# Kernel optimization log

Hardware: AMD Instinct MI355X
Metric: run time of the kernel (lower is better)

Reference implementation:

```python
import jax, jax.numpy as jnp
import numpy as np

BN_EPS = 1e-3  # keras BatchNormalization default epsilon

def _prelu(x, a):
    return jnp.maximum(x, 0) + a * jnp.minimum(x, 0)

def _bn(x, g, b, m, v):
    # inference-mode batchnorm with moving statistics
    return (x - m) * jax.lax.rsqrt(v + BN_EPS) * g + b

def setup_inputs() -> dict:
    key = jax.random.key(0)
    ks = jax.random.split(key, 24)
    B, D, V, L = 4096, 768, 200000, 200000
    F = 3 * D  # 2304 = qid|pos|neg concat
    n = lambda i, shape, s=0.05: jax.random.normal(ks[i], shape, jnp.float32) * s
    return dict(
        qid_embeddings=jax.random.normal(ks[0], (B, D), jnp.float32),
        node_embeddings=n(1, (V, D), 0.1),
        leaf_embeddings=n(2, (L, D), 0.1),
        positives=jax.random.randint(ks[3], (B,), 0, V),
        negetives=jax.random.randint(ks[4], (B,), 0, V),
        p_isleafs=jax.random.randint(ks[5], (B,), 0, 2),
        n_isleafs=jax.random.randint(ks[6], (B,), 0, 2),
        W00=n(7, (F, 36)), b00=jnp.zeros((36,)), a00=jnp.full((36,), 0.25),
        W01=n(8, (36, 1)), b01=jnp.zeros((1,)),
        W1=n(9, (F, 128)), b1=jnp.zeros((128,)), a1=jnp.full((128,), 0.25),
        g1=jnp.ones((128,)), be1=n(10, (128,), 0.1), m1=n(11, (128,), 0.1),
        v1=jax.random.uniform(ks[12], (128,)) + 0.5,
        W2=n(13, (128, 64)), b2=jnp.zeros((64,)), a2=jnp.full((64,), 0.25),
        g2=jnp.ones((64,)), be2=n(14, (64,), 0.1), m2=n(15, (64,), 0.1),
        v2=jax.random.uniform(ks[16], (64,)) + 0.5,
        W3=n(17, (64, 24)), b3=jnp.zeros((24,)), a3=jnp.full((24,), 0.25),
        g3=jnp.ones((24,)), be3=n(18, (24,), 0.1), m3=n(19, (24,), 0.1),
        v3=jax.random.uniform(ks[20], (24,)) + 0.5,
        W4=n(21, (24, 2)), b4=jnp.zeros((2,)),
    )

def reference(qid_embeddings, node_embeddings, leaf_embeddings, positives, negetives,
              p_isleafs, n_isleafs, W00, b00, a00, W01, b01,
              W1, b1, a1, g1, be1, m1, v1,
              W2, b2, a2, g2, be2, m2, v2,
              W3, b3, a3, g3, be3, m3, v3, W4, b4):
    # per-sample conditional embedding gather (leaf table vs internal node table)
    pos = jnp.where((p_isleafs == 1)[:, None], leaf_embeddings[positives], node_embeddings[positives])  # [B,D]
    neg = jnp.where((n_isleafs == 1)[:, None], leaf_embeddings[negetives], node_embeddings[negetives])  # [B,D]
    q = qid_embeddings  # [B,D]
    # attention block: small Dense(36)->Dense(1) scalar weight per sample
    feat = jnp.concatenate([q, pos, neg], axis=1)  # [B,3D]
    h = _prelu(feat @ W00 + b00, a00)              # [B,36]
    w = h @ W01 + b01                              # [B,1]
    item = jnp.concatenate([w * pos, w * neg, q], axis=1)  # [B,3D]
    # MLP 2304 -> 128 -> 64 -> 24 -> 2 (layer10/20/30 unused in original call)
    x = _bn(_prelu(item @ W1 + b1, a1), g1, be1, m1, v1)
    x = _bn(_prelu(x @ W2 + b2, a2), g2, be2, m2, v2)
    x = _bn(_prelu(x @ W3 + b3, a3), g3, be3, m3, v3)
    return jax.nn.softmax(x @ W4 + b4, axis=-1)  # [B,2]
```

## Files before the change

### kernel.cpp

```cpp
#include <hip/hip_runtime.h>
#include <hip/hip_bf16.h>

typedef _Float16 half8 __attribute__((ext_vector_type(8)));
typedef _Float16 half4v __attribute__((ext_vector_type(4)));
typedef float f32x4 __attribute__((ext_vector_type(4)));

#define NCOLS 176
#define TILE_ELEMS (NCOLS*32)
#define TILE_U16 (TILE_ELEMS/8)
#define WTSTR 40
#define XSTR2 2312
#define BM 16

#define BAR() do { asm volatile("s_waitcnt lgkmcnt(0)" ::: "memory"); \
  __builtin_amdgcn_s_barrier(); \
  __builtin_amdgcn_sched_barrier(0); } while (0)

#define OFF_A36 0
#define OFF_TQ  2560
#define OFF_TPN 10752
#define OFF_WV  18944
#define OFF_X1  19008
#define OFF_W2  27456
#define OFF_X2  43840
#define OFF_W3  48192
#define OFF_X3  51264
#define OFF_SCR 53056
#define SM_BYTES 77632

struct Params {
  const float *qid, *node, *leaf;
  const int *pos_idx, *neg_idx, *p_leaf, *n_leaf;
  const float *b00, *a00, *W01, *b01;
  const float *b1, *a1, *g1, *be1, *m1, *v1;
  const float *W2, *b2, *a2, *g2, *be2, *m2, *v2;
  const float *W3, *b3, *a3, *g3, *be3, *m3, *v3;
  const float *W4, *b4;
  const _Float16 *Wp;
  float *out;
};

__global__ __launch_bounds__(256) void pack_weights(const float* __restrict__ W00,
                                                    const float* __restrict__ W1,
                                                    _Float16* __restrict__ Wp) {
  int g = blockIdx.x;
  int s = g / 24, t = g - s * 24;
  int k0 = t * 32;
  int w1row0 = (s == 0) ? 1536 : (s == 1 ? 0 : 768);
  __shared__ _Float16 T[NCOLS][WTSTR];
  int tid = threadIdx.x;
  for (int u = tid; u < 1024; u += 256) {
    int kk = u >> 5, c4 = u & 31;
    float4 f = *(const float4*)(W1 + (size_t)(w1row0 + k0 + kk) * 128 + c4 * 4);
    int c = 48 + c4 * 4;
    T[c + 0][kk] = (_Float16)f.x; T[c + 1][kk] = (_Float16)f.y;
    T[c + 2][kk] = (_Float16)f.z; T[c + 3][kk] = (_Float16)f.w;
  }
  for (int u = tid; u < 1152; u += 256) {
    int kk = u / 36, c = u - kk * 36;
    T[c][kk] = (_Float16)W00[(size_t)(s * 768 + k0 + kk) * 36 + c];
  }
  for (int u = tid; u < 384; u += 256) {
    int kk = u & 31, c = 36 + (u >> 5);
    T[c][kk] = (_Float16)0.f;
  }
  __syncthreads();
  uint4* dst = (uint4*)(Wp + (size_t)g * TILE_ELEMS);
  for (int u = tid; u < TILE_U16; u += 256) {
    int c = u >> 2, q = u & 3;
    dst[u] = *(const uint4*)&T[c][q * 8];
  }
}

__global__ __launch_bounds__(512) void fused_main(Params p) {
  __shared__ __align__(16) char sm[SM_BYTES];
  __shared__ const float* Xbase[3][BM];

  _Float16* X   = (_Float16*)sm;
  float*    A36 = (float*)(sm + OFF_A36);
  float*    Tq  = (float*)(sm + OFF_TQ);
  float*    Tpn = (float*)(sm + OFF_TPN);
  float*    wv  = (float*)(sm + OFF_WV);
  float*    x1  = (float*)(sm + OFF_X1);
  _Float16* W2h = (_Float16*)(sm + OFF_W2);
  float*    x2  = (float*)(sm + OFF_X2);
  _Float16* W3h = (_Float16*)(sm + OFF_W3);
  float*    x3  = (float*)(sm + OFF_X3);
  float*    scr = (float*)(sm + OFF_SCR);

  const int tid  = threadIdx.x;
  const int wid  = tid >> 6;
  const int lane = tid & 63;
  const int lm   = lane & 15;
  const int hk   = lane >> 4;
  const int nw   = wid & 3;
  const int kg   = wid >> 2;
  const int m0   = blockIdx.x * BM;
  const bool HAS2 = (nw < 3);

  const uint4* Wp4 = (const uint4*)p.Wp;
  const int woff = ((nw * 48 + lm) << 2) + hk;

  uint4 P[4][3];
  auto ldWp = [&](int j) {
    int s = j / 12;
    int g = s * 24 + kg + 2 * (j - s * 12);
    const uint4* b = Wp4 + (size_t)g * TILE_U16 + woff;
    P[j & 3][0] = b[0]; P[j & 3][1] = b[64];
    if (HAS2) P[j & 3][2] = b[128];
  };

  ldWp(0); ldWp(1); ldWp(2); ldWp(3);

  if (tid < 3 * BM) {
    int s = tid >> 4, i = tid & 15;
    const float* base;
    if (s == 0) base = p.qid + (size_t)(m0 + i) * 768;
    else if (s == 1) {
      int idx = p.pos_idx[m0 + i];
      base = ((p.p_leaf[m0 + i] == 1) ? p.leaf : p.node) + (size_t)idx * 768;
    } else {
      int idx = p.neg_idx[m0 + i];
      base = ((p.n_leaf[m0 + i] == 1) ? p.leaf : p.node) + (size_t)idx * 768;
    }
    Xbase[s][i] = base;
  }

  float4 sregA[6], sregB[6], sregC[6];
  auto stageLoad = [&](int s, float4* sr) {
#pragma unroll
    for (int jj = 0; jj < 6; ++jj) {
      int v = tid + jj * 512;
      int i = v / 192, c4 = v - i * 192;
      const float* b = (s == 0) ? (p.qid + (size_t)(m0 + i) * 768) : Xbase[s][i];
      sr[jj] = ((const float4*)b)[c4];
    }
  };
  auto stageWrite = [&](int s, const float4* sr) {
#pragma unroll
    for (int jj = 0; jj < 6; ++jj) {
      int v = tid + jj * 512;
      int i = v / 192, c4 = v - i * 192;
      float4 f = sr[jj];
      half4v h = { (_Float16)f.x, (_Float16)f.y, (_Float16)f.z, (_Float16)f.w };
      *(half4v*)(X + i * XSTR2 + s * 768 + c4 * 4) = h;
    }
  };

  BAR();
  stageLoad(0, sregA);
  stageLoad(1, sregB);
  stageLoad(2, sregC);
  stageWrite(0, sregA);
  BAR();

  f32x4 accA[3] = {{0.f,0.f,0.f,0.f},{0.f,0.f,0.f,0.f},{0.f,0.f,0.f,0.f}};
  f32x4 accB[3] = {{0.f,0.f,0.f,0.f},{0.f,0.f,0.f,0.f},{0.f,0.f,0.f,0.f}};
  half8 av[3];

  auto ldA = [&](int g) -> half8 {
    return *(const half8*)(X + lm * XSTR2 + g * 32 + hk * 8);
  };
  auto comp = [&](int g, int slot, half8 a) {
    half8 b0 = __builtin_bit_cast(half8, P[slot][0]);
    half8 b1 = __builtin_bit_cast(half8, P[slot][1]);
    half8 b2 = __builtin_bit_cast(half8, P[slot][2]);
    if ((nw == 0) || (g < 24)) {
      accA[0] = __builtin_amdgcn_mfma_f32_16x16x32_f16(a, b0, accA[0], 0, 0, 0);
      accA[1] = __builtin_amdgcn_mfma_f32_16x16x32_f16(a, b1, accA[1], 0, 0, 0);
      if (HAS2) accA[2] = __builtin_amdgcn_mfma_f32_16x16x32_f16(a, b2, accA[2], 0, 0, 0);
    } else {
      accB[0] = __builtin_amdgcn_mfma_f32_16x16x32_f16(a, b0, accB[0], 0, 0, 0);
      accB[1] = __builtin_amdgcn_mfma_f32_16x16x32_f16(a, b1, accB[1], 0, 0, 0);
      if (HAS2) accB[2] = __builtin_amdgcn_mfma_f32_16x16x32_f16(a, b2, accB[2], 0, 0, 0);
    }
  };

  float4 w2r[4];
#pragma unroll
  for (int s = 0; s < 3; ++s) {
    if (s == 1) {
#pragma unroll
      for (int jj = 0; jj < 4; ++jj) w2r[jj] = ((const float4*)p.W2)[tid + jj * 512];
      stageWrite(1, sregB);
      BAR();
    }
    if (s == 2) {
      stageWrite(2, sregC);
      BAR();
    }
    const int gb = s * 24 + kg;
    av[0] = ldA(gb); av[1] = ldA(gb + 2); av[2] = ldA(gb + 4);
#pragma unroll
    for (int tt = 0; tt < 12; ++tt) {
      int j = s * 12 + tt;
      comp(gb + 2 * tt, j & 3, av[tt % 3]);
      if (j + 4 < 36) ldWp(j + 4);
      if (tt + 3 < 12) av[tt % 3] = ldA(gb + 2 * (tt + 3));
    }
  }

  BAR();
  if (kg == 1) {
#pragma unroll
    for (int n = 0; n < 3; ++n) {
      if (n < 2 || HAS2) {
#pragma unroll
        for (int r = 0; r < 4; ++r) {
          int base = ((nw * 3 + n) * 2) * 256 + (hk * 4 + r) * 16 + lm;
          scr[base]       = accA[n][r];
          scr[base + 256] = accB[n][r];
        }
      }
    }
  }
  BAR();
  if (kg == 0) {
#pragma unroll
    for (int n = 0; n < 3; ++n) {
      if (n < 2 || HAS2) {
#pragma unroll
        for (int r = 0; r < 4; ++r) {
          int base = ((nw * 3 + n) * 2) * 256 + (hk * 4 + r) * 16 + lm;
          float va = accA[n][r] + scr[base];
          float vb = accB[n][r] + scr[base + 256];
          int row = hk * 4 + r;
          int col = nw * 48 + n * 16 + lm;
          if (nw == 0) { if (col < 36) A36[row * 40 + col] = va; }
          else { int rc = col - 48; Tq[row * 128 + rc] = va; Tpn[row * 128 + rc] = vb; }
        }
      }
    }
  }
  BAR();

#pragma unroll
  for (int jj = 0; jj < 4; ++jj) {
    int u = tid + jj * 512;
    float4 f = w2r[jj];
    half4v h = { (_Float16)f.x, (_Float16)f.y, (_Float16)f.z, (_Float16)f.w };
    *(half4v*)(W2h + (u >> 4) * 64 + (u & 15) * 4) = h;
  }
  if (tid < BM) {
    float acc = p.b01[0];
    for (int c = 0; c < 36; ++c) {
      float h = A36[tid * 40 + c] + p.b00[c];
      h = (h > 0.f) ? h : p.a00[c] * h;
      acc += h * p.W01[c];
    }
    wv[tid] = acc;
  }
  BAR();

#pragma unroll
  for (int j = 0; j < 4; ++j) {
    int u = tid + j * 512;
    int i = u >> 7, c = u & 127;
    float v = wv[i] * Tpn[i * 128 + c] + Tq[i * 128 + c] + p.b1[c];
    v = (v > 0.f) ? v : p.a1[c] * v;
    v = (v - p.m1[c]) * (1.f / sqrtf(p.v1[c] + 1e-3f)) * p.g1[c] + p.be1[c];
    x1[i * 132 + c] = v;
  }
  BAR();

  if (tid < 256) {
    int i = tid & 15, cq = tid >> 4;
    const float* xr = x1 + i * 132;
    f32x4 acc0 = { p.b2[cq*4+0], p.b2[cq*4+1], p.b2[cq*4+2], p.b2[cq*4+3] };
    f32x4 acc1 = { 0.f, 0.f, 0.f, 0.f };
#pragma unroll 8
    for (int k = 0; k < 128; k += 2) {
      half4v w0 = *(const half4v*)(W2h + k * 64 + cq * 4);
      half4v w1 = *(const half4v*)(W2h + (k + 1) * 64 + cq * 4);
      acc0 += xr[k]     * __builtin_convertvector(w0, f32x4);
      acc1 += xr[k + 1] * __builtin_convertvector(w1, f32x4);
    }
    f32x4 acc = acc0 + acc1;
#pragma unroll
    for (int jj = 0; jj < 4; ++jj) {
      int c = cq * 4 + jj;
      float v = acc[jj];
      v = (v > 0.f) ? v : p.a2[c] * v;
      v = (v - p.m2[c]) * (1.f / sqrtf(p.v2[c] + 1e-3f)) * p.g2[c] + p.be2[c];
      x2[i * 68 + c] = v;
    }
  }
  for (int j = 0; j < 3; ++j) {
    int u = tid + j * 512;
    W3h[u] = (_Float16)p.W3[u];
  }
  BAR();

  if (tid < 384) {
    int i = tid & 15, c = tid >> 4;
    float acc = p.b3[c];
#pragma unroll 8
    for (int k = 0; k < 64; ++k) acc += x2[i * 68 + k] * (float)W3h[k * 24 + c];
    acc = (acc > 0.f) ? acc : p.a3[c] * acc;
    acc = (acc - p.m3[c]) * (1.f / sqrtf(p.v3[c] + 1e-3f)) * p.g3[c] + p.be3[c];
    x3[i * 28 + c] = acc;
  }
  BAR();

  if (tid < BM) {
    float l0 = p.b4[0], l1 = p.b4[1];
#pragma unroll
    for (int k = 0; k < 24; ++k) {
      float v = x3[tid * 28 + k];
      l0 += v * p.W4[k * 2 + 0];
      l1 += v * p.W4[k * 2 + 1];
    }
    float m = fmaxf(l0, l1);
    float e0 = __expf(l0 - m), e1 = __expf(l1 - m);
    float inv = 1.f / (e0 + e1);
    p.out[(size_t)(m0 + tid) * 2 + 0] = e0 * inv;
    p.out[(size_t)(m0 + tid) * 2 + 1] = e1 * inv;
  }
}

extern "C" void kernel_launch(void* const* d_in, const int* in_sizes, int n_in,
                              void* d_out, int out_size, void* d_ws, size_t ws_size,
                              hipStream_t stream) {
  const float* qid  = (const float*)d_in[0];
  const float* node = (const float*)d_in[1];
  const float* leaf = (const float*)d_in[2];
  const int* positives = (const int*)d_in[3];
  const int* negetives = (const int*)d_in[4];
  const int* p_isleafs = (const int*)d_in[5];
  const int* n_isleafs = (const int*)d_in[6];
  const float* W00 = (const float*)d_in[7];
  const float* b00 = (const float*)d_in[8];
  const float* a00 = (const float*)d_in[9];
  const float* W01 = (const float*)d_in[10];
  const float* b01 = (const float*)d_in[11];
  const float* W1  = (const float*)d_in[12];
  const float* b1  = (const float*)d_in[13];
  const float* a1  = (const float*)d_in[14];
  const float* g1  = (const float*)d_in[15];
  const float* be1 = (const float*)d_in[16];
  const float* m1  = (const float*)d_in[17];
  const float* v1  = (const float*)d_in[18];
  const float* W2  = (const float*)d_in[19];
  const float* b2  = (const float*)d_in[20];
  const float* a2  = (const float*)d_in[21];
  const float* g2  = (const float*)d_in[22];
  const float* be2 = (const float*)d_in[23];
  const float* m2  = (const float*)d_in[24];
  const float* v2  = (const float*)d_in[25];
  const float* W3  = (const float*)d_in[26];
  const float* b3  = (const float*)d_in[27];
  const float* a3  = (const float*)d_in[28];
  const float* g3  = (const float*)d_in[29];
  const float* be3 = (const float*)d_in[30];
  const float* m3  = (const float*)d_in[31];
  const float* v3  = (const float*)d_in[32];
  const float* W4  = (const float*)d_in[33];
  const float* b4  = (const float*)d_in[34];

  _Float16* Wp = (_Float16*)d_ws;

  pack_weights<<<72, 256, 0, stream>>>(W00, W1, Wp);

  Params p;
  p.qid = qid; p.node = node; p.leaf = leaf;
  p.pos_idx = positives; p.neg_idx = negetives; p.p_leaf = p_isleafs; p.n_leaf = n_isleafs;
  p.b00 = b00; p.a00 = a00; p.W01 = W01; p.b01 = b01;
  p.b1 = b1; p.a1 = a1; p.g1 = g1; p.be1 = be1; p.m1 = m1; p.v1 = v1;
  p.W2 = W2; p.b2 = b2; p.a2 = a2; p.g2 = g2; p.be2 = be2; p.m2 = m2; p.v2 = v2;
  p.W3 = W3; p.b3 = b3; p.a3 = a3; p.g3 = g3; p.be3 = be3; p.m3 = m3; p.v3 = v3;
  p.W4 = W4; p.b4 = b4;
  p.Wp = Wp;
  p.out = (float*)d_out;

  int B = in_sizes[3];
  fused_main<<<B / BM, 512, 0, stream>>>(p);
}
```

Baseline: 41.18 us.

## Use 768 threads with 3-way K split and double-buffered activation staging

Raises the block size from 512 to 768 threads, so each of three K-groups handles one third of the fused GEMM K range instead of two halves. The staged q/pos/neg rows go into two ping-pong LDS buffers and the next segment is written while the current one computes. The shared pointer table and the leading barrier are removed, and the sched_barrier is dropped from BAR. Fewer per-thread registers and more concurrent waves are meant to hide gather latency, at the cost of more LDS per block (which may lower occupancy) and an extra cross-group reduction.

```diff
diff --git a/kernel.cpp b/kernel.cpp
--- a/kernel.cpp
+++ b/kernel.cpp
@@ -9,12 +9,13 @@
 #define TILE_ELEMS (NCOLS*32)
 #define TILE_U16 (TILE_ELEMS/8)
 #define WTSTR 40
-#define XSTR2 2312
+#define XSTR 776
+#define XBUF_F16 12416
 #define BM 16
+#define NTHR 768
 
 #define BAR() do { asm volatile("s_waitcnt lgkmcnt(0)" ::: "memory"); \
-  __builtin_amdgcn_s_barrier(); \
-  __builtin_amdgcn_sched_barrier(0); } while (0)
+  __builtin_amdgcn_s_barrier(); } while (0)
 
 #define OFF_A36 0
 #define OFF_TQ  2560
@@ -25,8 +26,8 @@
 #define OFF_X2  43840
 #define OFF_W3  48192
 #define OFF_X3  51264
-#define OFF_SCR 53056
-#define SM_BYTES 77632
+#define OFF_SCR 49664
+#define SM_BYTES 98816
 
 struct Params {
   const float *qid, *node, *leaf;
@@ -72,9 +73,8 @@
   }
 }
 
-__global__ __launch_bounds__(512) void fused_main(Params p) {
+__global__ __launch_bounds__(NTHR) void fused_main(Params p) {
   __shared__ __align__(16) char sm[SM_BYTES];
-  __shared__ const float* Xbase[3][BM];
 
   _Float16* X   = (_Float16*)sm;
   float*    A36 = (float*)(sm + OFF_A36);
@@ -103,8 +103,8 @@
 
   uint4 P[4][3];
   auto ldWp = [&](int j) {
-    int s = j / 12;
-    int g = s * 24 + kg + 2 * (j - s * 12);
+    int s = j >> 3;
+    int g = s * 24 + kg + 3 * (j - s * 8);
     const uint4* b = Wp4 + (size_t)g * TILE_U16 + woff;
     P[j & 3][0] = b[0]; P[j & 3][1] = b[64];
     if (HAS2) P[j & 3][2] = b[128];
@@ -112,42 +112,33 @@
 
   ldWp(0); ldWp(1); ldWp(2); ldWp(3);
 
-  if (tid < 3 * BM) {
-    int s = tid >> 4, i = tid & 15;
-    const float* base;
-    if (s == 0) base = p.qid + (size_t)(m0 + i) * 768;
-    else if (s == 1) {
-      int idx = p.pos_idx[m0 + i];
-      base = ((p.p_leaf[m0 + i] == 1) ? p.leaf : p.node) + (size_t)idx * 768;
-    } else {
-      int idx = p.neg_idx[m0 + i];
-      base = ((p.n_leaf[m0 + i] == 1) ? p.leaf : p.node) + (size_t)idx * 768;
-    }
-    Xbase[s][i] = base;
-  }
-
-  float4 sregA[6], sregB[6], sregC[6];
+  auto rowbase = [&](int s, int i) -> const float* {
+    if (s == 0) return p.qid + (size_t)(m0 + i) * 768;
+    int idx = (s == 1 ? p.pos_idx : p.neg_idx)[m0 + i];
+    int lf  = (s == 1 ? p.p_leaf  : p.n_leaf )[m0 + i];
+    return ((lf == 1) ? p.leaf : p.node) + (size_t)idx * 768;
+  };
+
+  float4 sregA[4], sregB[4], sregC[4];
   auto stageLoad = [&](int s, float4* sr) {
 #pragma unroll
-    for (int jj = 0; jj < 6; ++jj) {
-      int v = tid + jj * 512;
+    for (int jj = 0; jj < 4; ++jj) {
+      int v = tid + jj * NTHR;
       int i = v / 192, c4 = v - i * 192;
-      const float* b = (s == 0) ? (p.qid + (size_t)(m0 + i) * 768) : Xbase[s][i];
-      sr[jj] = ((const float4*)b)[c4];
-    }
-  };
-  auto stageWrite = [&](int s, const float4* sr) {
-#pragma unroll
-    for (int jj = 0; jj < 6; ++jj) {
-      int v = tid + jj * 512;
+      sr[jj] = ((const float4*)rowbase(s, i))[c4];
+    }
+  };
+  auto stageWrite = [&](int dstbuf, const float4* sr) {
+#pragma unroll
+    for (int jj = 0; jj < 4; ++jj) {
+      int v = tid + jj * NTHR;
       int i = v / 192, c4 = v - i * 192;
       float4 f = sr[jj];
       half4v h = { (_Float16)f.x, (_Float16)f.y, (_Float16)f.z, (_Float16)f.w };
-      *(half4v*)(X + i * XSTR2 + s * 768 + c4 * 4) = h;
-    }
-  };
-
-  BAR();
+      *(half4v*)(X + dstbuf * XBUF_F16 + i * XSTR + c4 * 4) = h;
+    }
+  };
+
   stageLoad(0, sregA);
   stageLoad(1, sregB);
   stageLoad(2, sregC);
@@ -156,16 +147,15 @@
 
   f32x4 accA[3] = {{0.f,0.f,0.f,0.f},{0.f,0.f,0.f,0.f},{0.f,0.f,0.f,0.f}};
   f32x4 accB[3] = {{0.f,0.f,0.f,0.f},{0.f,0.f,0.f,0.f},{0.f,0.f,0.f,0.f}};
-  half8 av[3];
-
-  auto ldA = [&](int g) -> half8 {
-    return *(const half8*)(X + lm * XSTR2 + g * 32 + hk * 8);
-  };
-  auto comp = [&](int g, int slot, half8 a) {
+
+  auto ldA = [&](int pbuf, int off) -> half8 {
+    return *(const half8*)(X + pbuf * XBUF_F16 + lm * XSTR + off);
+  };
+  auto comp = [&](int s, int slot, half8 a) {
     half8 b0 = __builtin_bit_cast(half8, P[slot][0]);
     half8 b1 = __builtin_bit_cast(half8, P[slot][1]);
     half8 b2 = __builtin_bit_cast(half8, P[slot][2]);
-    if ((nw == 0) || (g < 24)) {
+    if ((nw == 0) || (s == 0)) {
       accA[0] = __builtin_amdgcn_mfma_f32_16x16x32_f16(a, b0, accA[0], 0, 0, 0);
       accA[1] = __builtin_amdgcn_mfma_f32_16x16x32_f16(a, b1, accA[1], 0, 0, 0);
       if (HAS2) accA[2] = __builtin_amdgcn_mfma_f32_16x16x32_f16(a, b2, accA[2], 0, 0, 0);
@@ -176,38 +166,41 @@
     }
   };
 
-  float4 w2r[4];
-#pragma unroll
-  for (int s = 0; s < 3; ++s) {
-    if (s == 1) {
-#pragma unroll
-      for (int jj = 0; jj < 4; ++jj) w2r[jj] = ((const float4*)p.W2)[tid + jj * 512];
-      stageWrite(1, sregB);
-      BAR();
-    }
-    if (s == 2) {
-      stageWrite(2, sregC);
-      BAR();
-    }
-    const int gb = s * 24 + kg;
-    av[0] = ldA(gb); av[1] = ldA(gb + 2); av[2] = ldA(gb + 4);
-#pragma unroll
-    for (int tt = 0; tt < 12; ++tt) {
-      int j = s * 12 + tt;
-      comp(gb + 2 * tt, j & 3, av[tt % 3]);
-      if (j + 4 < 36) ldWp(j + 4);
-      if (tt + 3 < 12) av[tt % 3] = ldA(gb + 2 * (tt + 3));
-    }
-  }
-
-  BAR();
-  if (kg == 1) {
+  auto runSeg = [&](int s, const float4* sr, int dstbuf) {
+    const int pbuf = s & 1;
+    half8 avA = ldA(pbuf, kg * 32 + hk * 8);
+    half8 avB = ldA(pbuf, (kg + 3) * 32 + hk * 8);
+#pragma unroll
+    for (int tt = 0; tt < 8; ++tt) {
+      int j = s * 8 + tt;
+      comp(s, j & 3, avA);
+      if (j + 4 < 24) ldWp(j + 4);
+      avA = avB;
+      if (tt + 2 < 8) avB = ldA(pbuf, (kg + 3 * (tt + 2)) * 32 + hk * 8);
+      if (sr && tt == 2) stageWrite(dstbuf, sr);
+    }
+  };
+
+  float4 w2r[3];
+  runSeg(0, sregB, 1);
+  BAR();
+  runSeg(1, sregC, 0);
+#pragma unroll
+  for (int jj = 0; jj < 3; ++jj) {
+    int u = tid + jj * NTHR;
+    if (u < 2048) w2r[jj] = ((const float4*)p.W2)[u];
+  }
+  BAR();
+  runSeg(2, nullptr, 0);
+
+  BAR();
+  if (kg > 0) {
 #pragma unroll
     for (int n = 0; n < 3; ++n) {
       if (n < 2 || HAS2) {
 #pragma unroll
         for (int r = 0; r < 4; ++r) {
-          int base = ((nw * 3 + n) * 2) * 256 + (hk * 4 + r) * 16 + lm;
+          int base = (((kg - 1) * 12 + nw * 3 + n) * 2) * 256 + (hk * 4 + r) * 16 + lm;
           scr[base]       = accA[n][r];
           scr[base + 256] = accB[n][r];
         }
@@ -221,9 +214,10 @@
       if (n < 2 || HAS2) {
 #pragma unroll
         for (int r = 0; r < 4; ++r) {
-          int base = ((nw * 3 + n) * 2) * 256 + (hk * 4 + r) * 16 + lm;
-          float va = accA[n][r] + scr[base];
-          float vb = accB[n][r] + scr[base + 256];
+          int b1i = ((nw * 3 + n) * 2) * 256 + (hk * 4 + r) * 16 + lm;
+          int b2i = ((12 + nw * 3 + n) * 2) * 256 + (hk * 4 + r) * 16 + lm;
+          float va = accA[n][r] + scr[b1i] + scr[b2i];
+          float vb = accB[n][r] + scr[b1i + 256] + scr[b2i + 256];
           int row = hk * 4 + r;
           int col = nw * 48 + n * 16 + lm;
           if (nw == 0) { if (col < 36) A36[row * 40 + col] = va; }
@@ -235,11 +229,13 @@
   BAR();
 
 #pragma unroll
-  for (int jj = 0; jj < 4; ++jj) {
-    int u = tid + jj * 512;
-    float4 f = w2r[jj];
-    half4v h = { (_Float16)f.x, (_Float16)f.y, (_Float16)f.z, (_Float16)f.w };
-    *(half4v*)(W2h + (u >> 4) * 64 + (u & 15) * 4) = h;
+  for (int jj = 0; jj < 3; ++jj) {
+    int u = tid + jj * NTHR;
+    if (u < 2048) {
+      float4 f = w2r[jj];
+      half4v h = { (_Float16)f.x, (_Float16)f.y, (_Float16)f.z, (_Float16)f.w };
+      *(half4v*)(W2h + (u >> 4) * 64 + (u & 15) * 4) = h;
+    }
   }
   if (tid < BM) {
     float acc = p.b01[0];
@@ -253,13 +249,15 @@
   BAR();
 
 #pragma unroll
-  for (int j = 0; j < 4; ++j) {
-    int u = tid + j * 512;
-    int i = u >> 7, c = u & 127;
-    float v = wv[i] * Tpn[i * 128 + c] + Tq[i * 128 + c] + p.b1[c];
-    v = (v > 0.f) ? v : p.a1[c] * v;
-    v = (v - p.m1[c]) * (1.f / sqrtf(p.v1[c] + 1e-3f)) * p.g1[c] + p.be1[c];
-    x1[i * 132 + c] = v;
+  for (int j = 0; j < 3; ++j) {
+    int u = tid + j * NTHR;
+    if (u < 2048) {
+      int i = u >> 7, c = u & 127;
+      float v = wv[i] * Tpn[i * 128 + c] + Tq[i * 128 + c] + p.b1[c];
+      v = (v > 0.f) ? v : p.a1[c] * v;
+      v = (v - p.m1[c]) * (1.f / sqrtf(p.v1[c] + 1e-3f)) * p.g1[c] + p.be1[c];
+      x1[i * 132 + c] = v;
+    }
   }
   BAR();
 
@@ -285,9 +283,9 @@
       x2[i * 68 + c] = v;
     }
   }
-  for (int j = 0; j < 3; ++j) {
-    int u = tid + j * 512;
-    W3h[u] = (_Float16)p.W3[u];
+  for (int j = 0; j < 2; ++j) {
+    int u = tid + j * NTHR;
+    if (u < 1536) W3h[u] = (_Float16)p.W3[u];
   }
   BAR();
 
@@ -373,5 +371,5 @@
   p.out = (float*)d_out;
 
   int B = in_sizes[3];
-  fused_main<<<B / BM, 512, 0, stream>>>(p);
+  fused_main<<<B / BM, NTHR, 0, stream>>>(p);
 }
```

Result: faster. 40.31 us (-2.1%).
